# Kernel tuning notes

Hardware: AMD Instinct MI355X
Metric: run time of the kernel (lower is better)

The kernel has to match this reference:

```python
import math
import jax, jax.numpy as jnp
import numpy as np

B, W_LEN, C = 4, 2048, 768
H = 3  # fixed number of heads in the module
K = C // H  # head dim


def setup_inputs() -> dict:
    key = jax.random.key(0)
    k1, k2, k3 = jax.random.split(key, 3)
    in_sequence_bwc = jax.random.normal(k1, (B, W_LEN, C), dtype=jnp.float32)
    # torch nn.Linear weights: [out_features, in_features], scaled for stability
    W_qkv = jax.random.normal(k2, (3 * C, C), dtype=jnp.float32) * (1.0 / math.sqrt(C))
    W_proj = jax.random.normal(k3, (C, C), dtype=jnp.float32) * (1.0 / math.sqrt(C))
    return {"in_sequence_bwc": in_sequence_bwc, "W_qkv": W_qkv, "W_proj": W_proj}


def reference(in_sequence_bwc, W_qkv, W_proj):
    batch, words, coords = in_sequence_bwc.shape
    head_dim = coords // H
    # qkv projection: x @ W^T  -> [b, w, 3c]
    all_bwd = jnp.einsum("bwc,dc->bwd", in_sequence_bwc, W_qkv)
    q_bwc, k_bwc, v_bwc = jnp.split(all_bwd, 3, axis=-1)
    # [b, h, w, k]
    q = q_bwc.reshape(batch, words, H, head_dim).transpose(0, 2, 1, 3)
    k = k_bwc.reshape(batch, words, H, head_dim).transpose(0, 2, 1, 3)
    v = v_bwc.reshape(batch, words, H, head_dim).transpose(0, 2, 1, 3)
    # scaled scores with causal mask -> softmax -> @V
    scores = jnp.einsum("bhqk,bhmk->bhqm", q, k) / math.sqrt(head_dim)
    causal = jnp.tril(jnp.ones((words, words), dtype=bool))
    scores = jnp.where(causal[None, None], scores, -jnp.inf)
    probs = jax.nn.softmax(scores, axis=-1)
    out = jnp.einsum("bhqm,bhmk->bhqk", probs, v)
    out_bwc = out.transpose(0, 2, 1, 3).reshape(batch, words, coords)
    return jnp.einsum("bwc,dc->bwd", out_bwc, W_proj)
```

## Files before the change

kernel.cpp:

```cpp
#include <hip/hip_runtime.h>

using v8h = __attribute__((ext_vector_type(8))) _Float16;
using v4f = __attribute__((ext_vector_type(4))) float;
using v4u = __attribute__((ext_vector_type(4))) unsigned short;
using v8u = __attribute__((ext_vector_type(8))) unsigned short;

__device__ __forceinline__ unsigned short f2h(float x) {
  _Float16 h = (_Float16)x;
  return __builtin_bit_cast(unsigned short, h);
}
__device__ __forceinline__ float h2f(unsigned short u) {
  return (float)__builtin_bit_cast(_Float16, u);
}

__device__ __forceinline__ void gl_lds16(const unsigned short* g, unsigned short* l) {
  __builtin_amdgcn_global_load_lds(
      (const __attribute__((address_space(1))) unsigned int*)g,
      (__attribute__((address_space(3))) unsigned int*)l, 16, 0, 0);
}

__global__ void cvt3_kernel(const float* __restrict__ X,
                            const float* __restrict__ Wq,
                            const float* __restrict__ Wp,
                            unsigned short* __restrict__ Xb,
                            unsigned short* __restrict__ Wqb,
                            unsigned short* __restrict__ Wpb) {
  const int blk = (int)blockIdx.x;
  const float* src;
  unsigned short* dst;
  int i;
  if (blk < 3072)      { src = X;  dst = Xb;  i = blk * 256 + threadIdx.x; }
  else if (blk < 3936) { src = Wq; dst = Wqb; i = (blk - 3072) * 256 + threadIdx.x; }
  else                 { src = Wp; dst = Wpb; i = (blk - 3936) * 256 + threadIdx.x; }
  const float* p = src + (size_t)i * 8;
  float4 a = *(const float4*)p;
  float4 b = *(const float4*)(p + 4);
  v8u o = {f2h(a.x), f2h(a.y), f2h(a.z), f2h(a.w),
           f2h(b.x), f2h(b.y), f2h(b.z), f2h(b.w)};
  *(v8u*)(dst + (size_t)i * 8) = o;
}

__global__ __launch_bounds__(512, 2)
void qkv8_kernel(const unsigned short* __restrict__ A,
                 const unsigned short* __restrict__ Bw,
                 unsigned short* __restrict__ QK) {
  __shared__ unsigned short sm[65536];
  const int t    = (int)threadIdx.x;
  const int ln   = t & 63;
  const int wv   = t >> 6;
  const int quad = ln >> 4;
  const int L    = ln & 15;
  const int wm   = wv >> 2;
  const int wn   = wv & 3;
  const long m0  = (long)blockIdx.y * 256;
  const long n0  = (long)blockIdx.x * 256;

  const int srow = t >> 3;
  const int scol = ((t & 7) ^ (srow & 7)) * 8;
  const unsigned short* Ath = A + (m0 + srow) * 768 + scol;
  const unsigned short* Bth = Bw + (n0 + srow) * 768 + scol;
  unsigned short* lth = &sm[t * 8];

  const int l7   = L & 7;
  const int sl0  = ((0 + quad) ^ l7) * 8;
  const int sl1  = ((4 + quad) ^ l7) * 8;
  const int arow = (wm * 128 + L) * 64;
  const int brow = (wn * 64 + L) * 64;

  v4f acc[8][4];
#pragma unroll
  for (int i = 0; i < 8; i++)
#pragma unroll
    for (int j = 0; j < 4; j++) acc[i][j] = (v4f){0.f, 0.f, 0.f, 0.f};

  auto stA = [&](int tile, int h) {
    if (tile >= 12) return;
    const unsigned short* g = Ath + (h * 128) * 768 + tile * 64;
    unsigned short* l = lth + (tile & 1) * 32768 + h * 8192;
    gl_lds16(g, l);
    gl_lds16(g + 64 * 768, l + 4096);
  };
  auto stB = [&](int tile, int h) {
    if (tile >= 12) return;
    const unsigned short* g = Bth + (h * 128) * 768 + tile * 64;
    unsigned short* l = lth + (tile & 1) * 32768 + 16384 + h * 8192;
    gl_lds16(g, l);
    gl_lds16(g + 64 * 768, l + 4096);
  };

  stB(0, 0); stB(0, 1); stA(0, 0); stA(0, 1);
  stB(1, 0); stB(1, 1); stA(1, 0);
  asm volatile("s_waitcnt vmcnt(6)" ::: "memory");
  __builtin_amdgcn_s_barrier();
  __builtin_amdgcn_sched_barrier(0);

#pragma unroll 2
  for (int kt = 0; kt < 12; ++kt) {
    const unsigned short* sA = &sm[(kt & 1) * 32768];
    const unsigned short* sB = sA + 16384;
    v8h af[4][2], b0[2][2], b1[2][2];

#pragma unroll
    for (int i = 0; i < 4; i++) {
      af[i][0] = *(const v8h*)&sA[arow + i * 1024 + sl0];
      af[i][1] = *(const v8h*)&sA[arow + i * 1024 + sl1];
    }
#pragma unroll
    for (int j = 0; j < 2; j++) {
      b0[j][0] = *(const v8h*)&sB[brow + j * 1024 + sl0];
      b0[j][1] = *(const v8h*)&sB[brow + j * 1024 + sl1];
    }
    stA(kt + 1, 1);
    __builtin_amdgcn_s_barrier();
    asm volatile("s_waitcnt lgkmcnt(0)" ::: "memory");
    __builtin_amdgcn_sched_barrier(0);
    __builtin_amdgcn_s_setprio(1);
#pragma unroll
    for (int i = 0; i < 4; i++)
#pragma unroll
      for (int j = 0; j < 2; j++) {
        acc[i][j] = __builtin_amdgcn_mfma_f32_16x16x32_f16(af[i][0], b0[j][0], acc[i][j], 0, 0, 0);
        acc[i][j] = __builtin_amdgcn_mfma_f32_16x16x32_f16(af[i][1], b0[j][1], acc[i][j], 0, 0, 0);
      }
    __builtin_amdgcn_s_setprio(0);
    __builtin_amdgcn_s_barrier();
    __builtin_amdgcn_sched_barrier(0);

#pragma unroll
    for (int j = 0; j < 2; j++) {
      b1[j][0] = *(const v8h*)&sB[brow + 2048 + j * 1024 + sl0];
      b1[j][1] = *(const v8h*)&sB[brow + 2048 + j * 1024 + sl1];
    }
    __builtin_amdgcn_s_barrier();
    asm volatile("s_waitcnt lgkmcnt(0)" ::: "memory");
    __builtin_amdgcn_sched_barrier(0);
    __builtin_amdgcn_s_setprio(1);
#pragma unroll
    for (int i = 0; i < 4; i++)
#pragma unroll
      for (int j = 0; j < 2; j++) {
        acc[i][2 + j] = __builtin_amdgcn_mfma_f32_16x16x32_f16(af[i][0], b1[j][0], acc[i][2 + j], 0, 0, 0);
        acc[i][2 + j] = __builtin_amdgcn_mfma_f32_16x16x32_f16(af[i][1], b1[j][1], acc[i][2 + j], 0, 0, 0);
      }
    __builtin_amdgcn_s_setprio(0);
    __builtin_amdgcn_s_barrier();
    __builtin_amdgcn_sched_barrier(0);

#pragma unroll
    for (int i = 0; i < 4; i++) {
      af[i][0] = *(const v8h*)&sA[arow + 4096 + i * 1024 + sl0];
      af[i][1] = *(const v8h*)&sA[arow + 4096 + i * 1024 + sl1];
    }
    stB(kt + 2, 0);
    __builtin_amdgcn_s_barrier();
    asm volatile("s_waitcnt lgkmcnt(0)" ::: "memory");
    __builtin_amdgcn_sched_barrier(0);
    __builtin_amdgcn_s_setprio(1);
#pragma unroll
    for (int i = 0; i < 4; i++)
#pragma unroll
      for (int j = 0; j < 2; j++) {
        acc[4 + i][2 + j] = __builtin_amdgcn_mfma_f32_16x16x32_f16(af[i][0], b1[j][0], acc[4 + i][2 + j], 0, 0, 0);
        acc[4 + i][2 + j] = __builtin_amdgcn_mfma_f32_16x16x32_f16(af[i][1], b1[j][1], acc[4 + i][2 + j], 0, 0, 0);
      }
    __builtin_amdgcn_s_setprio(0);
    __builtin_amdgcn_s_barrier();
    __builtin_amdgcn_sched_barrier(0);

    stB(kt + 2, 1);
    stA(kt + 2, 0);
    __builtin_amdgcn_s_barrier();
    __builtin_amdgcn_sched_barrier(0);
    __builtin_amdgcn_s_setprio(1);
#pragma unroll
    for (int i = 0; i < 4; i++)
#pragma unroll
      for (int j = 0; j < 2; j++) {
        acc[4 + i][j] = __builtin_amdgcn_mfma_f32_16x16x32_f16(af[i][0], b0[j][0], acc[4 + i][j], 0, 0, 0);
        acc[4 + i][j] = __builtin_amdgcn_mfma_f32_16x16x32_f16(af[i][1], b0[j][1], acc[4 + i][j], 0, 0, 0);
      }
    __builtin_amdgcn_s_setprio(0);
    if (kt + 2 < 12)      { asm volatile("s_waitcnt vmcnt(6)" ::: "memory"); }
    else if (kt + 1 < 12) { asm volatile("s_waitcnt vmcnt(0)" ::: "memory"); }
    __builtin_amdgcn_s_barrier();
    __builtin_amdgcn_sched_barrier(0);
  }

#pragma unroll
  for (int mi = 0; mi < 8; mi++) {
    const long row = m0 + wm * 128 + (mi >> 2) * 64 + (mi & 3) * 16 + quad * 4;
#pragma unroll
    for (int nj = 0; nj < 4; nj++) {
      const long col = n0 + wn * 64 + nj * 16 + L;
#pragma unroll
      for (int r = 0; r < 4; r++)
        QK[(row + r) * 1536 + col] = f2h(acc[mi][nj][r]);
    }
  }
}

__global__ __launch_bounds__(256, 2)
void gemm_proj_kernel(const unsigned short* __restrict__ A,
                      const unsigned short* __restrict__ Bw,
                      float* __restrict__ C) {
  __shared__ unsigned short As[4096];
  __shared__ unsigned short Bs[4096];

  const int t    = threadIdx.x;
  const int ln   = t & 63;
  const int wv   = t >> 6;
  const int quad = ln >> 4;
  const int L    = ln & 15;
  const int wm   = (wv >> 1) * 64;
  const int wn   = (wv & 1) * 64;
  const long m0  = (long)blockIdx.y * 128;
  const long n0  = (long)blockIdx.x * 128;

  v4f acc[4][4];
#pragma unroll
  for (int i = 0; i < 4; i++)
#pragma unroll
    for (int j = 0; j < 4; j++) acc[i][j] = (v4f){0.f, 0.f, 0.f, 0.f};

  const int ar = t >> 2;
  const int ac = (t & 3) * 8;
  const unsigned short* Ag = A + (m0 + ar) * 768 + ac;
  const unsigned short* Bg = Bw + (n0 + ar) * 768 + ac;
  unsigned short* la = &As[t * 8];
  unsigned short* lb = &Bs[t * 8];
  const long rowskip = 64L * 768;

  for (int k0 = 0; k0 < 768; k0 += 32) {
    gl_lds16(Ag + k0, la);
    gl_lds16(Ag + rowskip + k0, la + 2048);
    gl_lds16(Bg + k0, lb);
    gl_lds16(Bg + rowskip + k0, lb + 2048);
    __syncthreads();

    v8h af[4], bfr[4];
#pragma unroll
    for (int i = 0; i < 4; i++)
      af[i] = *(const v8h*)(&As[(wm + i * 16 + L) * 32 + quad * 8]);
#pragma unroll
    for (int j = 0; j < 4; j++)
      bfr[j] = *(const v8h*)(&Bs[(wn + j * 16 + L) * 32 + quad * 8]);
#pragma unroll
    for (int i = 0; i < 4; i++)
#pragma unroll
      for (int j = 0; j < 4; j++)
        acc[i][j] = __builtin_amdgcn_mfma_f32_16x16x32_f16(af[i], bfr[j], acc[i][j], 0, 0, 0);
    __syncthreads();
  }

#pragma unroll
  for (int i = 0; i < 4; i++)
#pragma unroll
    for (int j = 0; j < 4; j++)
#pragma unroll
      for (int r = 0; r < 4; r++) {
        long row = m0 + wm + i * 16 + quad * 4 + r;
        long col = n0 + wn + j * 16 + L;
        C[row * 768 + col] = acc[i][j][r];
      }
}

__global__ __launch_bounds__(256, 2)
void scv_kernel(const unsigned short* __restrict__ QK,
                const unsigned short* __restrict__ Xb,
                const unsigned short* __restrict__ Wq,
                unsigned short* __restrict__ Sc,
                unsigned short* __restrict__ VT) {
  __shared__ unsigned short As[4096];
  __shared__ unsigned short Bs[4096];

  const int t    = threadIdx.x;
  const int ln   = t & 63;
  const int wv   = t >> 6;
  const int quad = ln >> 4;
  const int L    = ln & 15;
  const int wm   = (wv >> 1) * 64;
  const int wn   = (wv & 1) * 64;
  const int ar   = t >> 2;
  const int ac   = (t & 3) * 8;

  const int x  = (int)blockIdx.x;
  const int bh = (int)blockIdx.y;
  const bool isV = (x >= 136);

  const unsigned short* Ag;
  const unsigned short* Bg;
  long rowstride;
  int Klen;
  int mt = 0, nt = 0;

  if (!isV) {
    int xx = x, i = 0;
    while (xx >= i + 1) { xx -= i + 1; i++; }
    const int j = xx;
    const int b = bh / 3, h = bh % 3;
    const long tokA = (long)b * 2048 + i * 128;
    const long tokB = (long)b * 2048 + j * 128;
    Ag = QK + (tokA + ar) * 1536 + h * 256 + ac;
    Bg = QK + (tokB + ar) * 1536 + 768 + h * 256 + ac;
    rowstride = 1536;
    Klen = 256;
  } else {
    const int vi = (x - 136) + 32 * bh;
    mt = vi & 63;
    nt = vi >> 6;
    Ag = Xb + ((long)mt * 128 + ar) * 768 + ac;
    Bg = Wq + ((long)(1536 + nt * 128) + ar) * 768 + ac;
    rowstride = 768;
    Klen = 768;
  }

  v4f acc[4][4];
#pragma unroll
  for (int ii = 0; ii < 4; ii++)
#pragma unroll
    for (int jj = 0; jj < 4; jj++) acc[ii][jj] = (v4f){0.f, 0.f, 0.f, 0.f};

  unsigned short* la = &As[t * 8];
  unsigned short* lb = &Bs[t * 8];
  const long rowskip = 64L * rowstride;

  for (int k0 = 0; k0 < Klen; k0 += 32) {
    gl_lds16(Ag + k0, la);
    gl_lds16(Ag + rowskip + k0, la + 2048);
    gl_lds16(Bg + k0, lb);
    gl_lds16(Bg + rowskip + k0, lb + 2048);
    __syncthreads();

    v8h af[4], bfr[4];
#pragma unroll
    for (int ii = 0; ii < 4; ii++)
      af[ii] = *(const v8h*)(&As[(wm + ii * 16 + L) * 32 + quad * 8]);
#pragma unroll
    for (int jj = 0; jj < 4; jj++)
      bfr[jj] = *(const v8h*)(&Bs[(wn + jj * 16 + L) * 32 + quad * 8]);
#pragma unroll
    for (int ii = 0; ii < 4; ii++)
#pragma unroll
      for (int jj = 0; jj < 4; jj++)
        acc[ii][jj] = __builtin_amdgcn_mfma_f32_16x16x32_f16(af[ii], bfr[jj], acc[ii][jj], 0, 0, 0);
    __syncthreads();
  }

  if (!isV) {
    unsigned short* Sb = Sc + ((long)bh * 136 + x) * 16384;
#pragma unroll
    for (int ii = 0; ii < 4; ii++)
#pragma unroll
      for (int jj = 0; jj < 4; jj++)
#pragma unroll
        for (int r = 0; r < 4; r++) {
          int row = wm + ii * 16 + quad * 4 + r;
          int col = wn + jj * 16 + L;
          Sb[row * 128 + col] = f2h(acc[ii][jj][r]);
        }
  } else {
#pragma unroll
    for (int ii = 0; ii < 4; ii++)
#pragma unroll
      for (int jj = 0; jj < 4; jj++) {
        const int colp = nt * 128 + wn + jj * 16 + L;
        const int h    = colp >> 8;
        const int d    = colp & 255;
        const long token = (long)mt * 128 + wm + ii * 16 + quad * 4;
        const int b  = (int)(token >> 11);
        const int tk = (int)(token & 2047);
        v4u val = {f2h(acc[ii][jj][0]), f2h(acc[ii][jj][1]),
                   f2h(acc[ii][jj][2]), f2h(acc[ii][jj][3])};
        *(v4u*)(&VT[((long)(b * 3 + h) * 256 + d) * 2048 + tk]) = val;
      }
  }
}

__global__ __launch_bounds__(256, 4)
void softmax_kernel(unsigned short* __restrict__ Sc) {
  const int tt   = threadIdx.x;
  const int wv   = tt >> 6;
  const int lane = tt & 63;
  const int bh   = (int)blockIdx.y;

  const int r = 2047 - ((int)blockIdx.x * 4 + wv);
  const int i = r >> 7;
  const int rowloc = r & 127;
  const long base = ((long)bh * 136 + (long)i * (i + 1) / 2) * 16384 + rowloc * 128;
  const int Lrow = (i + 1) * 128;
  const int nch = (i + 4) >> 2;

  float xs[4][8];
  float mx = -1e30f;
  for (int k = 0; k < nch; k++) {
    int c0 = k * 512 + lane * 8;
    if (c0 < Lrow) {
      int j = c0 >> 7;
      v8u v = *(const v8u*)(Sc + base + (long)j * 16384 + (c0 & 127));
#pragma unroll
      for (int e = 0; e < 8; e++) {
        float f = (c0 + e <= r) ? h2f(v[e]) * 0.0625f : -1e30f;
        xs[k][e] = f;
        mx = fmaxf(mx, f);
      }
    } else {
#pragma unroll
      for (int e = 0; e < 8; e++) xs[k][e] = -1e30f;
    }
  }
#pragma unroll
  for (int d = 1; d < 64; d <<= 1) mx = fmaxf(mx, __shfl_xor(mx, d));

  float sum = 0.f;
  for (int k = 0; k < nch; k++)
#pragma unroll
    for (int e = 0; e < 8; e++) {
      float ex = __expf(xs[k][e] - mx);
      xs[k][e] = ex;
      sum += ex;
    }
#pragma unroll
  for (int d = 1; d < 64; d <<= 1) sum += __shfl_xor(sum, d);
  const float inv = 1.0f / sum;

  for (int k = 0; k < nch; k++) {
    int c0 = k * 512 + lane * 8;
    if (c0 < Lrow) {
      int j = c0 >> 7;
      v8u o;
#pragma unroll
      for (int e = 0; e < 8; e++) o[e] = f2h(xs[k][e] * inv);
      *(v8u*)(Sc + base + (long)j * 16384 + (c0 & 127)) = o;
    }
  }
}

__global__ __launch_bounds__(256, 2)
void gemm_pv_kernel(const unsigned short* __restrict__ Sc,
                    const unsigned short* __restrict__ VT,
                    unsigned short* __restrict__ Pp) {
  __shared__ unsigned short As[4096];
  __shared__ unsigned short Bs[4096];

  const int t    = threadIdx.x;
  const int ln   = t & 63;
  const int wv   = t >> 6;
  const int quad = ln >> 4;
  const int L    = ln & 15;
  const int wm   = (wv >> 1) * 64;
  const int wn   = (wv & 1) * 64;

  const int ix  = (int)blockIdx.x;
  const int i   = 15 - (ix >> 2);
  const int nh  = (ix >> 1) & 1;
  const int par = ix & 1;
  const int bh  = (int)blockIdx.y;

  v4f acc[4][4];
#pragma unroll
  for (int ii = 0; ii < 4; ii++)
#pragma unroll
    for (int jj = 0; jj < 4; jj++) acc[ii][jj] = (v4f){0.f, 0.f, 0.f, 0.f};

  const int ar = t >> 2;
  const int ac = (t & 3) * 8;
  const unsigned short* Abase =
      Sc + ((long)bh * 136 + (long)i * (i + 1) / 2) * 16384 + ar * 128 + ac;
  const unsigned short* Bg =
      VT + ((long)bh * 256 + nh * 128 + ar) * 2048 + ac;
  unsigned short* la = &As[t * 8];
  unsigned short* lb = &Bs[t * 8];

  for (int j = par; j <= i; j += 2) {
    const unsigned short* Aj = Abase + (long)j * 16384;
    const unsigned short* Bj = Bg + j * 128;
#pragma unroll
    for (int k0 = 0; k0 < 128; k0 += 32) {
      gl_lds16(Aj + k0, la);
      gl_lds16(Aj + 64 * 128 + k0, la + 2048);
      gl_lds16(Bj + k0, lb);
      gl_lds16(Bj + 64 * 2048 + k0, lb + 2048);
      __syncthreads();

      v8h af[4], bfr[4];
#pragma unroll
      for (int ii = 0; ii < 4; ii++)
        af[ii] = *(const v8h*)(&As[(wm + ii * 16 + L) * 32 + quad * 8]);
#pragma unroll
      for (int jj = 0; jj < 4; jj++)
        bfr[jj] = *(const v8h*)(&Bs[(wn + jj * 16 + L) * 32 + quad * 8]);
#pragma unroll
      for (int ii = 0; ii < 4; ii++)
#pragma unroll
        for (int jj = 0; jj < 4; jj++)
          acc[ii][jj] = __builtin_amdgcn_mfma_f32_16x16x32_f16(af[ii], bfr[jj], acc[ii][jj], 0, 0, 0);
      __syncthreads();
    }
  }

  unsigned short* Pb = Pp + ((((long)bh * 16 + i) * 2 + nh) * 2 + par) * 16384;
#pragma unroll
  for (int ii = 0; ii < 4; ii++)
#pragma unroll
    for (int jj = 0; jj < 4; jj++)
#pragma unroll
      for (int r = 0; r < 4; r++) {
        int row = wm + ii * 16 + quad * 4 + r;
        int col = wn + jj * 16 + L;
        Pb[row * 128 + col] = f2h(acc[ii][jj][r]);
      }
}

__global__ __launch_bounds__(256, 4)
void pv_combine_kernel(const unsigned short* __restrict__ Pp,
                       unsigned short* __restrict__ AO) {
  const int i  = (int)blockIdx.x >> 1;
  const int nh = (int)blockIdx.x & 1;
  const int bh = (int)blockIdx.y;
  const int b  = bh / 3, h = bh % 3;

  const int tid = threadIdx.x;
  const int row = tid >> 1;
  const int cs  = (tid & 1) * 64;

  const unsigned short* P0 = Pp + ((((long)bh * 16 + i) * 2 + nh) * 2 + 0) * 16384 + row * 128 + cs;
  const unsigned short* P1 = P0 + 16384;
  unsigned short* Or = AO + ((long)b * 2048 + i * 128 + row) * 768 + h * 256 + nh * 128 + cs;
#pragma unroll
  for (int q = 0; q < 8; q++) {
    v8u a = *(const v8u*)(P0 + q * 8);
    v8u c = *(const v8u*)(P1 + q * 8);
    v8u o;
#pragma unroll
    for (int e = 0; e < 8; e++) o[e] = f2h(h2f(a[e]) + h2f(c[e]));
    *(v8u*)(Or + q * 8) = o;
  }
}

extern "C" void kernel_launch(void* const* d_in, const int* in_sizes, int n_in,
                              void* d_out, int out_size, void* d_ws, size_t ws_size,
                              hipStream_t stream) {
  const float* X     = (const float*)d_in[0];
  const float* Wqkv  = (const float*)d_in[1];
  const float* Wproj = (const float*)d_in[2];
  float* out = (float*)d_out;

  const size_t SZ_QK = (size_t)8192 * 1536 * 2;
  const size_t SZ_VT = (size_t)3072 * 2048 * 2;
  const size_t SZ_SC = (size_t)12 * 136 * 16384 * 2;
  const size_t SZ_AO = (size_t)8192 * 768 * 2;
  const size_t SZ_WQ = (size_t)2304 * 768 * 2;

  char* ws = (char*)d_ws;
  unsigned short* QKb = (unsigned short*)ws;
  unsigned short* Ppb = QKb;
  unsigned short* VTb = (unsigned short*)(ws + SZ_QK);
  unsigned short* Scb = (unsigned short*)(ws + SZ_QK + SZ_VT);
  unsigned short* AOb = (unsigned short*)(ws + SZ_QK + SZ_VT + SZ_SC);
  unsigned short* Xb  = AOb;
  unsigned short* Wqb = (unsigned short*)(ws + SZ_QK + SZ_VT + SZ_SC + SZ_AO);
  unsigned short* Wpb = (unsigned short*)(ws + SZ_QK + SZ_VT + SZ_SC + SZ_AO + SZ_WQ);

  dim3 blk(256, 1, 1);
  cvt3_kernel<<<dim3(4224, 1, 1), blk, 0, stream>>>(X, Wqkv, Wproj, Xb, Wqb, Wpb);
  qkv8_kernel<<<dim3(6, 32, 1), dim3(512, 1, 1), 0, stream>>>(Xb, Wqb, QKb);
  scv_kernel<<<dim3(168, 12, 1), blk, 0, stream>>>(QKb, Xb, Wqb, Scb, VTb);
  softmax_kernel<<<dim3(512, 12, 1), blk, 0, stream>>>(Scb);
  gemm_pv_kernel<<<dim3(64, 12, 1), blk, 0, stream>>>(Scb, VTb, Ppb);
  pv_combine_kernel<<<dim3(32, 12, 1), blk, 0, stream>>>(Ppb, AOb);
  gemm_proj_kernel<<<dim3(6, 64, 1), blk, 0, stream>>>(AOb, Wpb, out);
}
```

Before: 257.1 us.

## Replace scores/V GEMM kernel with 256x256 tiled, double-buffered 8-wave kernel

Result: faster. 243.6 us (-5.3%).

```diff
diff --git a/kernel.cpp b/kernel.cpp
--- a/kernel.cpp
+++ b/kernel.cpp
@@ -199,6 +199,215 @@
   }
 }
 
+__global__ __launch_bounds__(512, 2)
+void scv8_kernel(const unsigned short* __restrict__ QK,
+                 const unsigned short* __restrict__ Xb,
+                 const unsigned short* __restrict__ Wq,
+                 unsigned short* __restrict__ Sc,
+                 unsigned short* __restrict__ VT) {
+  __shared__ unsigned short sm[65536];
+  const int t    = (int)threadIdx.x;
+  const int ln   = t & 63;
+  const int wv   = t >> 6;
+  const int quad = ln >> 4;
+  const int L    = ln & 15;
+  const int wm   = wv >> 2;
+  const int wn   = wv & 3;
+
+  const int x = (int)blockIdx.x;
+  const bool isV = (x < 96);
+  int NT, Ihi = 0, Jhi = 0, bh = 0, mt = 0, nt = 0;
+  const unsigned short* Abase;
+  const unsigned short* Bbase;
+  long astr, bstr;
+
+  if (isV) {
+    mt = x & 31;
+    nt = x >> 5;
+    Abase = Xb + (long)mt * 256 * 768;
+    Bbase = Wq + (long)(1536 + nt * 256) * 768;
+    astr = 768; bstr = 768; NT = 12;
+  } else {
+    int s = x - 96;
+    bh = s / 36;
+    int slot = s % 36;
+    while (slot >= Ihi + 1) { slot -= Ihi + 1; Ihi++; }
+    Jhi = slot;
+    const int b = bh / 3, h = bh % 3;
+    Abase = QK + ((long)b * 2048 + Ihi * 256) * 1536 + h * 256;
+    Bbase = QK + ((long)b * 2048 + Jhi * 256) * 1536 + 768 + h * 256;
+    astr = 1536; bstr = 1536; NT = 4;
+  }
+
+  const int srow = t >> 3;
+  const int scol = ((t & 7) ^ (srow & 7)) * 8;
+  const unsigned short* Ath = Abase + (long)srow * astr + scol;
+  const unsigned short* Bth = Bbase + (long)srow * bstr + scol;
+  unsigned short* lth = &sm[t * 8];
+
+  const int l7   = L & 7;
+  const int sl0  = ((0 + quad) ^ l7) * 8;
+  const int sl1  = ((4 + quad) ^ l7) * 8;
+  const int arow = (wm * 128 + L) * 64;
+  const int brow = (wn * 64 + L) * 64;
+
+  v4f acc[8][4];
+#pragma unroll
+  for (int i = 0; i < 8; i++)
+#pragma unroll
+    for (int j = 0; j < 4; j++) acc[i][j] = (v4f){0.f, 0.f, 0.f, 0.f};
+
+  auto stA = [&](int tile, int h) {
+    if (tile >= NT) return;
+    const unsigned short* g = Ath + (long)(h * 128) * astr + tile * 64;
+    unsigned short* l = lth + (tile & 1) * 32768 + h * 8192;
+    gl_lds16(g, l);
+    gl_lds16(g + 64 * astr, l + 4096);
+  };
+  auto stB = [&](int tile, int h) {
+    if (tile >= NT) return;
+    const unsigned short* g = Bth + (long)(h * 128) * bstr + tile * 64;
+    unsigned short* l = lth + (tile & 1) * 32768 + 16384 + h * 8192;
+    gl_lds16(g, l);
+    gl_lds16(g + 64 * bstr, l + 4096);
+  };
+
+  stB(0, 0); stB(0, 1); stA(0, 0); stA(0, 1);
+  stB(1, 0); stB(1, 1); stA(1, 0);
+  asm volatile("s_waitcnt vmcnt(6)" ::: "memory");
+  __builtin_amdgcn_s_barrier();
+  __builtin_amdgcn_sched_barrier(0);
+
+#pragma unroll 2
+  for (int kt = 0; kt < NT; ++kt) {
+    const unsigned short* sA = &sm[(kt & 1) * 32768];
+    const unsigned short* sB = sA + 16384;
+    v8h af[4][2], b0[2][2], b1[2][2];
+
+#pragma unroll
+    for (int i = 0; i < 4; i++) {
+      af[i][0] = *(const v8h*)&sA[arow + i * 1024 + sl0];
+      af[i][1] = *(const v8h*)&sA[arow + i * 1024 + sl1];
+    }
+#pragma unroll
+    for (int j = 0; j < 2; j++) {
+      b0[j][0] = *(const v8h*)&sB[brow + j * 1024 + sl0];
+      b0[j][1] = *(const v8h*)&sB[brow + j * 1024 + sl1];
+    }
+    stA(kt + 1, 1);
+    __builtin_amdgcn_s_barrier();
+    asm volatile("s_waitcnt lgkmcnt(0)" ::: "memory");
+    __builtin_amdgcn_sched_barrier(0);
+    __builtin_amdgcn_s_setprio(1);
+#pragma unroll
+    for (int i = 0; i < 4; i++)
+#pragma unroll
+      for (int j = 0; j < 2; j++) {
+        acc[i][j] = __builtin_amdgcn_mfma_f32_16x16x32_f16(af[i][0], b0[j][0], acc[i][j], 0, 0, 0);
+        acc[i][j] = __builtin_amdgcn_mfma_f32_16x16x32_f16(af[i][1], b0[j][1], acc[i][j], 0, 0, 0);
+      }
+    __builtin_amdgcn_s_setprio(0);
+    __builtin_amdgcn_s_barrier();
+    __builtin_amdgcn_sched_barrier(0);
+
+#pragma unroll
+    for (int j = 0; j < 2; j++) {
+      b1[j][0] = *(const v8h*)&sB[brow + 2048 + j * 1024 + sl0];
+      b1[j][1] = *(const v8h*)&sB[brow + 2048 + j * 1024 + sl1];
+    }
+    __builtin_amdgcn_s_barrier();
+    asm volatile("s_waitcnt lgkmcnt(0)" ::: "memory");
+    __builtin_amdgcn_sched_barrier(0);
+    __builtin_amdgcn_s_setprio(1);
+#pragma unroll
+    for (int i = 0; i < 4; i++)
+#pragma unroll
+      for (int j = 0; j < 2; j++) {
+        acc[i][2 + j] = __builtin_amdgcn_mfma_f32_16x16x32_f16(af[i][0], b1[j][0], acc[i][2 + j], 0, 0, 0);
+        acc[i][2 + j] = __builtin_amdgcn_mfma_f32_16x16x32_f16(af[i][1], b1[j][1], acc[i][2 + j], 0, 0, 0);
+      }
+    __builtin_amdgcn_s_setprio(0);
+    __builtin_amdgcn_s_barrier();
+    __builtin_amdgcn_sched_barrier(0);
+
+#pragma unroll
+    for (int i = 0; i < 4; i++) {
+      af[i][0] = *(const v8h*)&sA[arow + 4096 + i * 1024 + sl0];
+      af[i][1] = *(const v8h*)&sA[arow + 4096 + i * 1024 + sl1];
+    }
+    stB(kt + 2, 0);
+    __builtin_amdgcn_s_barrier();
+    asm volatile("s_waitcnt lgkmcnt(0)" ::: "memory");
+    __builtin_amdgcn_sched_barrier(0);
+    __builtin_amdgcn_s_setprio(1);
+#pragma unroll
+    for (int i = 0; i < 4; i++)
+#pragma unroll
+      for (int j = 0; j < 2; j++) {
+        acc[4 + i][2 + j] = __builtin_amdgcn_mfma_f32_16x16x32_f16(af[i][0], b1[j][0], acc[4 + i][2 + j], 0, 0, 0);
+        acc[4 + i][2 + j] = __builtin_amdgcn_mfma_f32_16x16x32_f16(af[i][1], b1[j][1], acc[4 + i][2 + j], 0, 0, 0);
+      }
+    __builtin_amdgcn_s_setprio(0);
+    __builtin_amdgcn_s_barrier();
+    __builtin_amdgcn_sched_barrier(0);
+
+    stB(kt + 2, 1);
+    stA(kt + 2, 0);
+    __builtin_amdgcn_s_barrier();
+    __builtin_amdgcn_sched_barrier(0);
+    __builtin_amdgcn_s_setprio(1);
+#pragma unroll
+    for (int i = 0; i < 4; i++)
+#pragma unroll
+      for (int j = 0; j < 2; j++) {
+        acc[4 + i][j] = __builtin_amdgcn_mfma_f32_16x16x32_f16(af[i][0], b0[j][0], acc[4 + i][j], 0, 0, 0);
+        acc[4 + i][j] = __builtin_amdgcn_mfma_f32_16x16x32_f16(af[i][1], b0[j][1], acc[4 + i][j], 0, 0, 0);
+      }
+    __builtin_amdgcn_s_setprio(0);
+    if (kt + 2 < NT)      { asm volatile("s_waitcnt vmcnt(6)" ::: "memory"); }
+    else if (kt + 1 < NT) { asm volatile("s_waitcnt vmcnt(0)" ::: "memory"); }
+    __builtin_amdgcn_s_barrier();
+    __builtin_amdgcn_sched_barrier(0);
+  }
+
+  if (isV) {
+#pragma unroll
+    for (int mi = 0; mi < 8; mi++) {
+      const long token = (long)mt * 256 + wm * 128 + (mi >> 2) * 64 + (mi & 3) * 16 + quad * 4;
+      const int b  = (int)(token >> 11);
+      const int tk = (int)(token & 2047);
+#pragma unroll
+      for (int nj = 0; nj < 4; nj++) {
+        const int colp = nt * 256 + wn * 64 + nj * 16 + L;
+        const int h    = colp >> 8;
+        const int d    = colp & 255;
+        v4u val = {f2h(acc[mi][nj][0]), f2h(acc[mi][nj][1]),
+                   f2h(acc[mi][nj][2]), f2h(acc[mi][nj][3])};
+        *(v4u*)(&VT[((long)(b * 3 + h) * 256 + d) * 2048 + tk]) = val;
+      }
+    }
+  } else {
+    const int di = wm;
+    const int dj = wn >> 1;
+    const int i128 = 2 * Ihi + di;
+    const int j128 = 2 * Jhi + dj;
+    if (j128 <= i128) {
+      unsigned short* Sb = Sc + ((long)bh * 136 + (long)i128 * (i128 + 1) / 2 + j128) * 16384;
+#pragma unroll
+      for (int mi = 0; mi < 8; mi++) {
+        const int subrow = (mi >> 2) * 64 + (mi & 3) * 16 + quad * 4;
+#pragma unroll
+        for (int nj = 0; nj < 4; nj++) {
+          const int subcol = (wn & 1) * 64 + nj * 16 + L;
+#pragma unroll
+          for (int r = 0; r < 4; r++)
+            Sb[(subrow + r) * 128 + subcol] = f2h(acc[mi][nj][r]);
+        }
+      }
+    }
+  }
+}
+
 __global__ __launch_bounds__(256, 2)
 void gemm_proj_kernel(const unsigned short* __restrict__ A,
                       const unsigned short* __restrict__ Bw,
@@ -264,118 +473,6 @@
       }
 }
 
-__global__ __launch_bounds__(256, 2)
-void scv_kernel(const unsigned short* __restrict__ QK,
-                const unsigned short* __restrict__ Xb,
-                const unsigned short* __restrict__ Wq,
-                unsigned short* __restrict__ Sc,
-                unsigned short* __restrict__ VT) {
-  __shared__ unsigned short As[4096];
-  __shared__ unsigned short Bs[4096];
-
-  const int t    = threadIdx.x;
-  const int ln   = t & 63;
-  const int wv   = t >> 6;
-  const int quad = ln >> 4;
-  const int L    = ln & 15;
-  const int wm   = (wv >> 1) * 64;
-  const int wn   = (wv & 1) * 64;
-  const int ar   = t >> 2;
-  const int ac   = (t & 3) * 8;
-
-  const int x  = (int)blockIdx.x;
-  const int bh = (int)blockIdx.y;
-  const bool isV = (x >= 136);
-
-  const unsigned short* Ag;
-  const unsigned short* Bg;
-  long rowstride;
-  int Klen;
-  int mt = 0, nt = 0;
-
-  if (!isV) {
-    int xx = x, i = 0;
-    while (xx >= i + 1) { xx -= i + 1; i++; }
-    const int j = xx;
-    const int b = bh / 3, h = bh % 3;
-    const long tokA = (long)b * 2048 + i * 128;
-    const long tokB = (long)b * 2048 + j * 128;
-    Ag = QK + (tokA + ar) * 1536 + h * 256 + ac;
-    Bg = QK + (tokB + ar) * 1536 + 768 + h * 256 + ac;
-    rowstride = 1536;
-    Klen = 256;
-  } else {
-    const int vi = (x - 136) + 32 * bh;
-    mt = vi & 63;
-    nt = vi >> 6;
-    Ag = Xb + ((long)mt * 128 + ar) * 768 + ac;
-    Bg = Wq + ((long)(1536 + nt * 128) + ar) * 768 + ac;
-    rowstride = 768;
-    Klen = 768;
-  }
-
-  v4f acc[4][4];
-#pragma unroll
-  for (int ii = 0; ii < 4; ii++)
-#pragma unroll
-    for (int jj = 0; jj < 4; jj++) acc[ii][jj] = (v4f){0.f, 0.f, 0.f, 0.f};
-
-  unsigned short* la = &As[t * 8];
-  unsigned short* lb = &Bs[t * 8];
-  const long rowskip = 64L * rowstride;
-
-  for (int k0 = 0; k0 < Klen; k0 += 32) {
-    gl_lds16(Ag + k0, la);
-    gl_lds16(Ag + rowskip + k0, la + 2048);
-    gl_lds16(Bg + k0, lb);
-    gl_lds16(Bg + rowskip + k0, lb + 2048);
-    __syncthreads();
-
-    v8h af[4], bfr[4];
-#pragma unroll
-    for (int ii = 0; ii < 4; ii++)
-      af[ii] = *(const v8h*)(&As[(wm + ii * 16 + L) * 32 + quad * 8]);
-#pragma unroll
-    for (int jj = 0; jj < 4; jj++)
-      bfr[jj] = *(const v8h*)(&Bs[(wn + jj * 16 + L) * 32 + quad * 8]);
-#pragma unroll
-    for (int ii = 0; ii < 4; ii++)
-#pragma unroll
-      for (int jj = 0; jj < 4; jj++)
-        acc[ii][jj] = __builtin_amdgcn_mfma_f32_16x16x32_f16(af[ii], bfr[jj], acc[ii][jj], 0, 0, 0);
-    __syncthreads();
-  }
-
-  if (!isV) {
-    unsigned short* Sb = Sc + ((long)bh * 136 + x) * 16384;
-#pragma unroll
-    for (int ii = 0; ii < 4; ii++)
-#pragma unroll
-      for (int jj = 0; jj < 4; jj++)
-#pragma unroll
-        for (int r = 0; r < 4; r++) {
-          int row = wm + ii * 16 + quad * 4 + r;
-          int col = wn + jj * 16 + L;
-          Sb[row * 128 + col] = f2h(acc[ii][jj][r]);
-        }
-  } else {
-#pragma unroll
-    for (int ii = 0; ii < 4; ii++)
-#pragma unroll
-      for (int jj = 0; jj < 4; jj++) {
-        const int colp = nt * 128 + wn + jj * 16 + L;
-        const int h    = colp >> 8;
-        const int d    = colp & 255;
-        const long token = (long)mt * 128 + wm + ii * 16 + quad * 4;
-        const int b  = (int)(token >> 11);
-        const int tk = (int)(token & 2047);
-        v4u val = {f2h(acc[ii][jj][0]), f2h(acc[ii][jj][1]),
-                   f2h(acc[ii][jj][2]), f2h(acc[ii][jj][3])};
-        *(v4u*)(&VT[((long)(b * 3 + h) * 256 + d) * 2048 + tk]) = val;
-      }
-  }
-}
-
 __global__ __launch_bounds__(256, 4)
 void softmax_kernel(unsigned short* __restrict__ Sc) {
   const int tt   = threadIdx.x;
@@ -564,7 +661,7 @@
   dim3 blk(256, 1, 1);
   cvt3_kernel<<<dim3(4224, 1, 1), blk, 0, stream>>>(X, Wqkv, Wproj, Xb, Wqb, Wpb);
   qkv8_kernel<<<dim3(6, 32, 1), dim3(512, 1, 1), 0, stream>>>(Xb, Wqb, QKb);
-  scv_kernel<<<dim3(168, 12, 1), blk, 0, stream>>>(QKb, Xb, Wqb, Scb, VTb);
+  scv8_kernel<<<dim3(528, 1, 1), dim3(512, 1, 1), 0, stream>>>(QKb, Xb, Wqb, Scb, VTb);
   softmax_kernel<<<dim3(512, 12, 1), blk, 0, stream>>>(Scb);
   gemm_pv_kernel<<<dim3(64, 12, 1), blk, 0, stream>>>(Scb, VTb, Ppb);
   pv_combine_kernel<<<dim3(32, 12, 1), blk, 0, stream>>>(Ppb, AOb);
```
